# Performance work log

Hardware: AMD Instinct MI355X
Metric: run time of the kernel (lower is better)

Reference implementation:

```python
import jax, jax.numpy as jnp
import numpy as np

N_NODES = 1_000_000
N_UPD = 131_072
H = 128        # memory_dim
D_MSG = 256    # message_dim


def setup_inputs() -> dict:
    key = jax.random.key(0)
    ks = jax.random.split(key, 7)
    s_ih = 1.0 / np.sqrt(H)
    return {
        "memory": jax.random.normal(ks[0], (N_NODES, H), dtype=jnp.float32),
        "node_ids": jax.random.randint(ks[1], (N_UPD,), 0, N_NODES),
        "messages": jax.random.normal(ks[2], (N_UPD, D_MSG), dtype=jnp.float32),
        "W_ih": jax.random.uniform(ks[3], (3 * H, D_MSG), minval=-s_ih, maxval=s_ih, dtype=jnp.float32),
        "W_hh": jax.random.uniform(ks[4], (3 * H, H), minval=-s_ih, maxval=s_ih, dtype=jnp.float32),
        "b_ih": jax.random.uniform(ks[5], (3 * H,), minval=-s_ih, maxval=s_ih, dtype=jnp.float32),
        "b_hh": jax.random.uniform(ks[6], (3 * H,), minval=-s_ih, maxval=s_ih, dtype=jnp.float32),
    }


def _gru_cell(x, h, W_ih, W_hh, b_ih, b_hh):
    # torch GRUCell math. gates laid out as [r, z, n] along dim 0 of weights.
    gi = x @ W_ih.T + b_ih            # [M, 3H]
    gh = h @ W_hh.T + b_hh            # [M, 3H]
    i_r, i_z, i_n = jnp.split(gi, 3, axis=-1)
    h_r, h_z, h_n = jnp.split(gh, 3, axis=-1)
    r = jax.nn.sigmoid(i_r + h_r)
    z = jax.nn.sigmoid(i_z + h_z)
    n = jnp.tanh(i_n + r * h_n)
    return (1.0 - z) * n + z * h


def reference(memory, node_ids, messages, W_ih, W_hh, b_ih, b_hh):
    node_mem = memory[node_ids]                              # gather [M, H]
    updated = _gru_cell(messages, node_mem, W_ih, W_hh, b_ih, b_hh)
    return memory.at[node_ids].set(updated)                  # scatter back into full table
```

## Files before the change

### kernel.cpp

```cpp
#include <hip/hip_runtime.h>
#include <math.h>

#define NN     1000000
#define NUPD   131072
#define HDIM   128
#define DMSG   256

#define GRU_ROWS    32
#define GRU_BLOCKS  (NUPD / GRU_ROWS)
#define COPY_BLOCKS 8192
#define TOTAL_BLOCKS (GRU_BLOCKS + COPY_BLOCKS)
#define COPY_STRIDE  ((long long)COPY_BLOCKS * 512)
#define COPY_ITERS   8
#define N4_TOTAL     ((long long)NN * (HDIM / 4))

#define WI_OFF  0
#define WH_OFF  (384 * 256 * 2)
#define WIN_OFF (WH_OFF + 384 * 128 * 2)

typedef __attribute__((ext_vector_type(8))) short bf16x8;
typedef __attribute__((ext_vector_type(4))) float f32x4;

__device__ __forceinline__ short f2bf(float f) {
  unsigned u = __float_as_uint(f);
  unsigned r = (u + 0x7fffu + ((u >> 16) & 1u)) >> 16;
  return (short)r;
}
__device__ __forceinline__ float sigmoidf_fast(float x) {
  return 1.0f / (1.0f + __expf(-x));
}
__device__ __forceinline__ float tanhf_fast(float x) {
  return 1.0f - 2.0f / (__expf(2.0f * x) + 1.0f);
}

__global__ void prep_kernel(const int* __restrict__ ids,
                            const float* __restrict__ Wi,
                            const float* __restrict__ Wh,
                            short* __restrict__ wi_bf,
                            short* __restrict__ wh_bf,
                            int* __restrict__ winner) {
  int i = blockIdx.x * 256 + threadIdx.x;
  if (i < NUPD) atomicMax(&winner[ids[i]], i);
  if (i < 384 * 256) wi_bf[i] = f2bf(Wi[i]);
  int j = i - 384 * 256;
  if (j >= 0 && j < 384 * 128) wh_bf[j] = f2bf(Wh[j]);
}

__launch_bounds__(512, 6)
__global__ void fat_kernel(const float* __restrict__ memory,
                           const int* __restrict__ node_ids,
                           const float* __restrict__ messages,
                           const short* __restrict__ Wi_bf,
                           const short* __restrict__ Wh_bf,
                           const float* __restrict__ b_ih,
                           const float* __restrict__ b_hh,
                           const int* __restrict__ winner,
                           float* __restrict__ out)
{
  __shared__ short xs[GRU_ROWS][DMSG + 8];
  __shared__ short hs[GRU_ROWS][HDIM + 8];
  __shared__ int   ids_s[GRU_ROWS];
  __shared__ char  flag_s[GRU_ROWS];

  const int tid = threadIdx.x;

  if (blockIdx.x >= GRU_BLOCKS) {
    const int ci = blockIdx.x - GRU_BLOCKS;
    const float4* __restrict__ src4 = (const float4*)memory;
    float4* __restrict__ dst4 = (float4*)out;
    const long long base = (long long)ci * 512 + tid;

    int w[COPY_ITERS];
#pragma unroll
    for (int it = 0; it < COPY_ITERS; ++it) {
      long long i = base + (long long)it * COPY_STRIDE;
      w[it] = (i < N4_TOTAL) ? winner[(int)(i >> 5)] : 0;
    }
#pragma unroll
    for (int it = 0; it < COPY_ITERS; ++it) {
      long long i = base + (long long)it * COPY_STRIDE;
      if (i < N4_TOTAL && w[it] < 0) dst4[i] = src4[i];
    }
    return;
  }

  const int row0 = blockIdx.x * GRU_ROWS;
  const int lane = tid & 63;
  const int wv   = tid >> 6;

  if (tid < GRU_ROWS) {
    int id = node_ids[row0 + tid];
    ids_s[tid] = id;
    flag_s[tid] = (winner[id] == row0 + tid) ? 1 : 0;
  }

  {
    int r = tid >> 4;
    int c16 = (tid & 15) * 16;
    const float4* p4 = (const float4*)(messages + (size_t)(row0 + r) * DMSG + c16);
    float4 v0 = p4[0], v1 = p4[1], v2 = p4[2], v3 = p4[3];
    bf16x8 o0, o1;
    o0[0] = f2bf(v0.x); o0[1] = f2bf(v0.y); o0[2] = f2bf(v0.z); o0[3] = f2bf(v0.w);
    o0[4] = f2bf(v1.x); o0[5] = f2bf(v1.y); o0[6] = f2bf(v1.z); o0[7] = f2bf(v1.w);
    o1[0] = f2bf(v2.x); o1[1] = f2bf(v2.y); o1[2] = f2bf(v2.z); o1[3] = f2bf(v2.w);
    o1[4] = f2bf(v3.x); o1[5] = f2bf(v3.y); o1[6] = f2bf(v3.z); o1[7] = f2bf(v3.w);
    *(bf16x8*)&xs[r][c16]     = o0;
    *(bf16x8*)&xs[r][c16 + 8] = o1;
  }

  {
    int r = tid >> 4;
    int c8 = (tid & 15) * 8;
    int id = node_ids[row0 + r];
    const float4* p4 = (const float4*)(memory + (size_t)id * HDIM + c8);
    float4 v0 = p4[0], v1 = p4[1];
    bf16x8 o;
    o[0] = f2bf(v0.x); o[1] = f2bf(v0.y); o[2] = f2bf(v0.z); o[3] = f2bf(v0.w);
    o[4] = f2bf(v1.x); o[5] = f2bf(v1.y); o[6] = f2bf(v1.z); o[7] = f2bf(v1.w);
    *(bf16x8*)&hs[r][c8] = o;
  }

  __syncthreads();

  const int g0  = __builtin_amdgcn_readfirstlane(wv * 16);
  const int col = lane & 15;
  const int kg  = lane >> 4;
  const int g   = g0 + col;

  f32x4 acc_r[2]  = {{0,0,0,0},{0,0,0,0}};
  f32x4 acc_z[2]  = {{0,0,0,0},{0,0,0,0}};
  f32x4 acc_in[2] = {{0,0,0,0},{0,0,0,0}};
  f32x4 acc_hn[2] = {{0,0,0,0},{0,0,0,0}};

#pragma unroll
  for (int ks = 0; ks < 8; ++ks) {
    const int ko = ks * 32 + kg * 8;
    bf16x8 br = *(const bf16x8*)(Wi_bf + (size_t)(g)       * DMSG + ko);
    bf16x8 bz = *(const bf16x8*)(Wi_bf + (size_t)(g + 128) * DMSG + ko);
    bf16x8 bn = *(const bf16x8*)(Wi_bf + (size_t)(g + 256) * DMSG + ko);
#pragma unroll
    for (int rt = 0; rt < 2; ++rt) {
      bf16x8 a = *(const bf16x8*)&xs[rt * 16 + col][ko];
      acc_r[rt]  = __builtin_amdgcn_mfma_f32_16x16x32_bf16(a, br, acc_r[rt], 0, 0, 0);
      acc_z[rt]  = __builtin_amdgcn_mfma_f32_16x16x32_bf16(a, bz, acc_z[rt], 0, 0, 0);
      acc_in[rt] = __builtin_amdgcn_mfma_f32_16x16x32_bf16(a, bn, acc_in[rt], 0, 0, 0);
    }
  }

#pragma unroll
  for (int ks = 0; ks < 4; ++ks) {
    const int ko = ks * 32 + kg * 8;
    bf16x8 br = *(const bf16x8*)(Wh_bf + (size_t)(g)       * HDIM + ko);
    bf16x8 bz = *(const bf16x8*)(Wh_bf + (size_t)(g + 128) * HDIM + ko);
    bf16x8 bn = *(const bf16x8*)(Wh_bf + (size_t)(g + 256) * HDIM + ko);
#pragma unroll
    for (int rt = 0; rt < 2; ++rt) {
      bf16x8 a = *(const bf16x8*)&hs[rt * 16 + col][ko];
      acc_r[rt]  = __builtin_amdgcn_mfma_f32_16x16x32_bf16(a, br, acc_r[rt], 0, 0, 0);
      acc_z[rt]  = __builtin_amdgcn_mfma_f32_16x16x32_bf16(a, bz, acc_z[rt], 0, 0, 0);
      acc_hn[rt] = __builtin_amdgcn_mfma_f32_16x16x32_bf16(a, bn, acc_hn[rt], 0, 0, 0);
    }
  }

  const float bias_r  = b_ih[g]       + b_hh[g];
  const float bias_z  = b_ih[g + 128] + b_hh[g + 128];
  const float bias_in = b_ih[g + 256];
  const float bias_hn = b_hh[g + 256];

#pragma unroll
  for (int rt = 0; rt < 2; ++rt) {
#pragma unroll
    for (int reg = 0; reg < 4; ++reg) {
      const int row = rt * 16 + kg * 4 + reg;
      const int id  = ids_s[row];
      float r = sigmoidf_fast(acc_r[rt][reg] + bias_r);
      float z = sigmoidf_fast(acc_z[rt][reg] + bias_z);
      float n = tanhf_fast(acc_in[rt][reg] + bias_in + r * (acc_hn[rt][reg] + bias_hn));
      float h = memory[(size_t)id * HDIM + g];
      float nh = (1.0f - z) * n + z * h;
      if (flag_s[row]) out[(size_t)id * HDIM + g] = nh;
    }
  }
}

extern "C" void kernel_launch(void* const* d_in, const int* in_sizes, int n_in,
                              void* d_out, int out_size, void* d_ws, size_t ws_size,
                              hipStream_t stream) {
  const float* memory   = (const float*)d_in[0];
  const int*   node_ids = (const int*)  d_in[1];
  const float* messages = (const float*)d_in[2];
  const float* W_ih     = (const float*)d_in[3];
  const float* W_hh     = (const float*)d_in[4];
  const float* b_ih     = (const float*)d_in[5];
  const float* b_hh     = (const float*)d_in[6];
  float* out = (float*)d_out;

  char* ws = (char*)d_ws;
  short* Wi_bf  = (short*)(ws + WI_OFF);
  short* Wh_bf  = (short*)(ws + WH_OFF);
  int*   winner = (int*)  (ws + WIN_OFF);

  hipMemsetAsync(winner, 0xFF, (size_t)NN * sizeof(int), stream);
  prep_kernel<<<(384 * 256 + 384 * 128 + 255) / 256, 256, 0, stream>>>(
      node_ids, W_ih, W_hh, Wi_bf, Wh_bf, winner);

  fat_kernel<<<TOTAL_BLOCKS, 512, 0, stream>>>(
      memory, node_ids, messages, Wi_bf, Wh_bf, b_ih, b_hh, winner, out);
}
```

Measured before the change: 359.9 us.

## Split fused copy/GRU kernel into separate full-table copy and GRU kernels

Removes the winner-masked copy branch from the fused kernel. A separate grid-stride kernel now copies the whole memory table unconditionally, and a dedicated GRU kernel then overwrites the updated rows. This drops the per-element winner reads and lets the GRU kernel use a higher occupancy launch bound. The cost is that the updated rows get written twice, and the copy and GRU work now run serially instead of overlapping.

```diff
diff --git a/kernel.cpp b/kernel.cpp
--- a/kernel.cpp
+++ b/kernel.cpp
@@ -8,11 +8,7 @@
 
 #define GRU_ROWS    32
 #define GRU_BLOCKS  (NUPD / GRU_ROWS)
-#define COPY_BLOCKS 8192
-#define TOTAL_BLOCKS (GRU_BLOCKS + COPY_BLOCKS)
-#define COPY_STRIDE  ((long long)COPY_BLOCKS * 512)
-#define COPY_ITERS   8
-#define N4_TOTAL     ((long long)NN * (HDIM / 4))
+#define N4_TOTAL    ((long long)NN * (HDIM / 4))
 
 #define WI_OFF  0
 #define WH_OFF  (384 * 256 * 2)
@@ -46,8 +42,15 @@
   if (j >= 0 && j < 384 * 128) wh_bf[j] = f2bf(Wh[j]);
 }
 
-__launch_bounds__(512, 6)
-__global__ void fat_kernel(const float* __restrict__ memory,
+__global__ void copy_kernel(const float4* __restrict__ src,
+                            float4* __restrict__ dst) {
+  long long i = (long long)blockIdx.x * blockDim.x + threadIdx.x;
+  const long long stride = (long long)gridDim.x * blockDim.x;
+  for (; i < N4_TOTAL; i += stride) dst[i] = src[i];
+}
+
+__launch_bounds__(512, 8)
+__global__ void gru_kernel(const float* __restrict__ memory,
                            const int* __restrict__ node_ids,
                            const float* __restrict__ messages,
                            const short* __restrict__ Wi_bf,
@@ -62,28 +65,7 @@
   __shared__ int   ids_s[GRU_ROWS];
   __shared__ char  flag_s[GRU_ROWS];
 
-  const int tid = threadIdx.x;
-
-  if (blockIdx.x >= GRU_BLOCKS) {
-    const int ci = blockIdx.x - GRU_BLOCKS;
-    const float4* __restrict__ src4 = (const float4*)memory;
-    float4* __restrict__ dst4 = (float4*)out;
-    const long long base = (long long)ci * 512 + tid;
-
-    int w[COPY_ITERS];
-#pragma unroll
-    for (int it = 0; it < COPY_ITERS; ++it) {
-      long long i = base + (long long)it * COPY_STRIDE;
-      w[it] = (i < N4_TOTAL) ? winner[(int)(i >> 5)] : 0;
-    }
-#pragma unroll
-    for (int it = 0; it < COPY_ITERS; ++it) {
-      long long i = base + (long long)it * COPY_STRIDE;
-      if (i < N4_TOTAL && w[it] < 0) dst4[i] = src4[i];
-    }
-    return;
-  }
-
+  const int tid  = threadIdx.x;
   const int row0 = blockIdx.x * GRU_ROWS;
   const int lane = tid & 63;
   const int wv   = tid >> 6;
@@ -204,6 +186,8 @@
   prep_kernel<<<(384 * 256 + 384 * 128 + 255) / 256, 256, 0, stream>>>(
       node_ids, W_ih, W_hh, Wi_bf, Wh_bf, winner);
 
-  fat_kernel<<<TOTAL_BLOCKS, 512, 0, stream>>>(
+  copy_kernel<<<4096, 512, 0, stream>>>((const float4*)memory, (float4*)out);
+
+  gru_kernel<<<GRU_BLOCKS, 512, 0, stream>>>(
       memory, node_ids, messages, Wi_bf, Wh_bf, b_ih, b_hh, winner, out);
 }
```

Measured after the change: 401.8 us. +11.6%, slower.

## Interleave copy and GRU blocks, contiguous copy chunks, keep fp32 h in LDS

Applied to the files above, without the earlier changes.

Copy blocks now each handle a contiguous chunk of 5×512 float4s, with all loads issued before the stores. Copy and GRU blocks are interleaved by block index so memory-bound copy work overlaps compute-bound MFMA work across the GPU. The fp32 gathered memory row is also kept in shared memory, so the epilogue no longer re-reads it from global memory. This adds about 17 KB of LDS per block, which may reduce occupancy for the GRU blocks.

```diff
diff --git a/kernel.cpp b/kernel.cpp
--- a/kernel.cpp
+++ b/kernel.cpp
@@ -8,11 +8,10 @@
 
 #define GRU_ROWS    32
 #define GRU_BLOCKS  (NUPD / GRU_ROWS)
-#define COPY_BLOCKS 8192
+#define COPY_BLOCKS 12500
+#define COPY_ITERS  5
+#define CHUNK       (COPY_ITERS * 512)
 #define TOTAL_BLOCKS (GRU_BLOCKS + COPY_BLOCKS)
-#define COPY_STRIDE  ((long long)COPY_BLOCKS * 512)
-#define COPY_ITERS   8
-#define N4_TOTAL     ((long long)NN * (HDIM / 4))
 
 #define WI_OFF  0
 #define WH_OFF  (384 * 256 * 2)
@@ -59,32 +58,45 @@
 {
   __shared__ short xs[GRU_ROWS][DMSG + 8];
   __shared__ short hs[GRU_ROWS][HDIM + 8];
+  __shared__ float hf[GRU_ROWS][HDIM + 4];
   __shared__ int   ids_s[GRU_ROWS];
   __shared__ char  flag_s[GRU_ROWS];
 
   const int tid = threadIdx.x;
-
-  if (blockIdx.x >= GRU_BLOCKS) {
-    const int ci = blockIdx.x - GRU_BLOCKS;
+  const int bid = blockIdx.x;
+
+  bool is_copy;
+  int ci = 0, gi = 0;
+  if (bid < 2 * GRU_BLOCKS) {
+    is_copy = (bid & 1);
+    if (is_copy) ci = bid >> 1; else gi = bid >> 1;
+  } else {
+    is_copy = true;
+    ci = GRU_BLOCKS + (bid - 2 * GRU_BLOCKS);
+  }
+
+  if (is_copy) {
     const float4* __restrict__ src4 = (const float4*)memory;
     float4* __restrict__ dst4 = (float4*)out;
-    const long long base = (long long)ci * 512 + tid;
+    const long long base = (long long)ci * CHUNK + tid;
 
     int w[COPY_ITERS];
 #pragma unroll
-    for (int it = 0; it < COPY_ITERS; ++it) {
-      long long i = base + (long long)it * COPY_STRIDE;
-      w[it] = (i < N4_TOTAL) ? winner[(int)(i >> 5)] : 0;
-    }
-#pragma unroll
-    for (int it = 0; it < COPY_ITERS; ++it) {
-      long long i = base + (long long)it * COPY_STRIDE;
-      if (i < N4_TOTAL && w[it] < 0) dst4[i] = src4[i];
-    }
+    for (int it = 0; it < COPY_ITERS; ++it)
+      w[it] = winner[(int)((base + (long long)it * 512) >> 5)];
+
+    float4 v[COPY_ITERS];
+#pragma unroll
+    for (int it = 0; it < COPY_ITERS; ++it)
+      v[it] = src4[base + (long long)it * 512];
+
+#pragma unroll
+    for (int it = 0; it < COPY_ITERS; ++it)
+      if (w[it] < 0) dst4[base + (long long)it * 512] = v[it];
     return;
   }
 
-  const int row0 = blockIdx.x * GRU_ROWS;
+  const int row0 = gi * GRU_ROWS;
   const int lane = tid & 63;
   const int wv   = tid >> 6;
 
@@ -118,6 +130,8 @@
     o[0] = f2bf(v0.x); o[1] = f2bf(v0.y); o[2] = f2bf(v0.z); o[3] = f2bf(v0.w);
     o[4] = f2bf(v1.x); o[5] = f2bf(v1.y); o[6] = f2bf(v1.z); o[7] = f2bf(v1.w);
     *(bf16x8*)&hs[r][c8] = o;
+    *(float4*)&hf[r][c8]     = v0;
+    *(float4*)&hf[r][c8 + 4] = v1;
   }
 
   __syncthreads();
@@ -176,7 +190,7 @@
       float r = sigmoidf_fast(acc_r[rt][reg] + bias_r);
       float z = sigmoidf_fast(acc_z[rt][reg] + bias_z);
       float n = tanhf_fast(acc_in[rt][reg] + bias_in + r * (acc_hn[rt][reg] + bias_hn));
-      float h = memory[(size_t)id * HDIM + g];
+      float h = hf[row][g];
       float nh = (1.0f - z) * n + z * h;
       if (flag_s[row]) out[(size_t)id * HDIM + g] = nh;
     }
```

Result: slower. 436.8 us (+21.4%).
